# Kernel tuning notes

Hardware: AMD Instinct MI355X
Metric: run time of the kernel (lower is better)

Reference implementation:

```python
import jax, jax.numpy as jnp
import numpy as np

N = 50000   # nodes
E = 800000  # edges before self-loops
H = 4       # heads
D = 64      # num_h_feats (per-head out dim of hidden layers)
C = 2       # num_classes
NEG = 0.2   # DGL GATConv leaky_relu negative_slope
EPS = 1e-5  # BatchNorm eps


def setup_inputs() -> dict:
    key = jax.random.key(0)
    ks = jax.random.split(key, 16)
    inp = {}
    inp['feats'] = jax.random.normal(ks[0], (N, 9), jnp.float32)
    inp['W1'] = jax.random.normal(ks[1], (9, H * D), jnp.float32) * 0.1
    inp['al1'] = jax.random.normal(ks[2], (H, D), jnp.float32) * 0.1
    inp['ar1'] = jax.random.normal(ks[3], (H, D), jnp.float32) * 0.1
    inp['b1'] = jnp.zeros((H, D), jnp.float32)
    inp['Wm'] = jax.random.normal(ks[4], (D, H * D), jnp.float32) * 0.1
    inp['alm'] = jax.random.normal(ks[5], (H, D), jnp.float32) * 0.1
    inp['arm'] = jax.random.normal(ks[6], (H, D), jnp.float32) * 0.1
    inp['bm'] = jnp.zeros((H, D), jnp.float32)
    inp['W2'] = jax.random.normal(ks[7], (D, H * C), jnp.float32) * 0.1
    inp['al2'] = jax.random.normal(ks[8], (H, C), jnp.float32) * 0.1
    inp['ar2'] = jax.random.normal(ks[9], (H, C), jnp.float32) * 0.1
    inp['b2'] = jnp.zeros((H, C), jnp.float32)
    inp['gamma'] = jnp.ones((D,), jnp.float32)
    inp['beta'] = jnp.zeros((D,), jnp.float32)
    inp['src'] = jax.random.randint(ks[10], (E,), 0, N, jnp.int32)
    inp['dst'] = jax.random.randint(ks[11], (E,), 0, N, jnp.int32)
    return inp


def gat_layer(x, W, al, ar, b, src, dst, out_d):
    """DGL GATConv: linear -> per-edge attention -> dst-softmax -> scatter-sum."""
    n = x.shape[0]
    z = (x @ W).reshape(n, H, out_d)                 # [N, H, Dout]
    el = jnp.sum(z * al, axis=-1)                    # [N, H] attn on src
    er = jnp.sum(z * ar, axis=-1)                    # [N, H] attn on dst
    e = jax.nn.leaky_relu(el[src] + er[dst], NEG)    # [E, H]
    m = jax.ops.segment_max(e, dst, num_segments=n)  # per-dst max (stable softmax)
    a = jnp.exp(e - m[dst])
    s = jax.ops.segment_sum(a, dst, num_segments=n)
    alpha = a / s[dst]                               # [E, H]
    out = jax.ops.segment_sum(alpha[:, :, None] * z[src], dst, num_segments=n)
    return out + b                                   # [N, H, Dout]


def batchnorm(h, gamma, beta):
    mu = jnp.mean(h, axis=0)
    var = jnp.var(h, axis=0)
    return (h - mu) * jax.lax.rsqrt(var + EPS) * gamma + beta


def reference(feats, W1, al1, ar1, b1, Wm, alm, arm, bm, W2, al2, ar2, b2,
              gamma, beta, src, dst):
    # dgl.add_self_loop
    loop = jnp.arange(N, dtype=src.dtype)
    s = jnp.concatenate([src, loop])
    d = jnp.concatenate([dst, loop])
    h = gat_layer(feats, W1, al1, ar1, b1, s, d, D).sum(axis=1)  # head-sum
    h = batchnorm(h, gamma, beta)
    h = gat_layer(h, Wm, alm, arm, bm, s, d, D).sum(axis=1)
    h = batchnorm(h, gamma, beta)
    o = gat_layer(h, W2, al2, ar2, b2, s, d, C).sum(axis=1)      # [N, C]
    return o
```

## Files before the change

### kernel.cpp

```cpp
#include <hip/hip_runtime.h>
#include <hip/hip_bf16.h>

typedef __hip_bfloat16 bf16;
typedef __bf16 bf16x8 __attribute__((ext_vector_type(8)));
typedef float f32x4 __attribute__((ext_vector_type(4)));
typedef _Float16 h16;
typedef _Float16 h16x4 __attribute__((ext_vector_type(4)));

__device__ __forceinline__ float b2f(bf16 v) { return __bfloat162float(v); }

__device__ __forceinline__ float ldin(const void* p, size_t i, int isb) {
    return isb ? b2f(((const bf16*)p)[i]) : ((const float*)p)[i];
}
__device__ __forceinline__ unsigned short f2bfbits(float f) {
    bf16 v = __float2bfloat16(f);
    return *(unsigned short*)&v;
}

__global__ __launch_bounds__(256) void prep_kernel(
    const void* __restrict__ feats, const void* __restrict__ W1, const void* __restrict__ Wm,
    const void* __restrict__ al1, const void* __restrict__ ar1,
    const void* __restrict__ alm, const void* __restrict__ arm,
    const unsigned* __restrict__ gbits,
    unsigned short* __restrict__ fpad, unsigned short* __restrict__ W1T,
    unsigned short* __restrict__ WmT,
    float* __restrict__ alf1, float* __restrict__ arf1,
    float* __restrict__ alfm, float* __restrict__ arfm,
    int* __restrict__ flag, int Nn) {
    int isb = (gbits[0] == 0x3F803F80u) ? 1 : 0;
    long t = (long)blockIdx.x * 256 + threadIdx.x;
    if (t == 0) *flag = isb;
    long n64 = (long)Nn * 64;
    if (t < n64) {
        int k = (int)(t & 63); long n = t >> 6;
        fpad[t] = (k < 9) ? f2bfbits(ldin(feats, (size_t)n * 9 + k, isb)) : 0;
    } else if (t < n64 + 16384) {
        long u = t - n64; int n = (int)(u >> 6), k = (int)(u & 63);
        W1T[u] = (k < 9) ? f2bfbits(ldin(W1, (size_t)k * 256 + n, isb)) : 0;
    } else if (t < n64 + 32768) {
        long u = t - n64 - 16384; int n = (int)(u >> 6), k = (int)(u & 63);
        WmT[u] = f2bfbits(ldin(Wm, (size_t)k * 256 + n, isb));
    } else if (t < n64 + 32768 + 256) {
        int u = (int)(t - n64 - 32768);
        alf1[u] = ldin(al1, u, isb); arf1[u] = ldin(ar1, u, isb);
        alfm[u] = ldin(alm, u, isb); arfm[u] = ldin(arm, u, isb);
    }
}

__global__ __launch_bounds__(256) void count_kernel(
    const int* __restrict__ dst, int* __restrict__ deg, int E) {
    int t = blockIdx.x * 256 + threadIdx.x;
    if (t < E) atomicAdd(&deg[dst[t]], 1);
}

__global__ __launch_bounds__(256) void scan1_kernel(
    const int* __restrict__ deg, int* __restrict__ off, int* __restrict__ bsum, int Nn) {
    __shared__ int s[256];
    int t = threadIdx.x, i = blockIdx.x * 256 + t;
    int v = (i < Nn) ? deg[i] : 0;
    s[t] = v; __syncthreads();
#pragma unroll
    for (int o = 1; o < 256; o <<= 1) {
        int a = (t >= o) ? s[t - o] : 0;
        __syncthreads();
        s[t] += a;
        __syncthreads();
    }
    if (i < Nn) off[i] = s[t];
    if (t == 255) bsum[blockIdx.x] = s[255];
}

__global__ __launch_bounds__(256) void scan2_kernel(int* __restrict__ bsum, int NB) {
    __shared__ int s[256];
    int t = threadIdx.x;
    int v = (t < NB) ? bsum[t] : 0;
    s[t] = v; __syncthreads();
#pragma unroll
    for (int o = 1; o < 256; o <<= 1) {
        int a = (t >= o) ? s[t - o] : 0;
        __syncthreads();
        s[t] += a;
        __syncthreads();
    }
    if (t < NB) bsum[t] = s[t] - v;
}

__global__ __launch_bounds__(256) void scan3_kernel(
    const int* __restrict__ deg, int* __restrict__ off, int* __restrict__ cur,
    const int* __restrict__ bsum, int Nn, int E) {
    int i = blockIdx.x * 256 + threadIdx.x;
    if (i < Nn) {
        int ex = off[i] - deg[i] + bsum[i >> 8];
        off[i] = ex;
        cur[i] = ex;
    }
    if (i == 0) off[Nn] = E;
}

__global__ __launch_bounds__(256) void scatter_kernel(
    const int* __restrict__ src, const int* __restrict__ dst,
    int* __restrict__ cur, int* __restrict__ adj, int E) {
    int t = blockIdx.x * 256 + threadIdx.x;
    if (t < E) {
        int p = atomicAdd(&cur[dst[t]], 1);
        adj[p] = src[t];
    }
}

__global__ __launch_bounds__(256) void lin_mfma_l1_kernel(
    const unsigned short* __restrict__ xb, const unsigned short* __restrict__ WT,
    const float* __restrict__ alf, const float* __restrict__ arf,
    h16* __restrict__ zh, float* __restrict__ el, float* __restrict__ er, int Nn) {
    __shared__ h16 zs[16 * 256];
    int w = threadIdx.x >> 6;
    int l = threadIdx.x & 63;
    int quad = l >> 4, lc = l & 15;
    int node0 = blockIdx.x * 16;

    int mrow = node0 + lc; if (mrow >= Nn) mrow = Nn - 1;
    const bf16x8* xa = (const bf16x8*)(xb + (size_t)mrow * 64);
    bf16x8 a0 = xa[quad];
    bf16x8 a1 = xa[quad + 4];

    float pe[4] = {0.f, 0.f, 0.f, 0.f}, pr[4] = {0.f, 0.f, 0.f, 0.f};
    int row0 = quad * 4;
#pragma unroll
    for (int ct = 0; ct < 4; ++ct) {
        int col = w * 64 + ct * 16 + lc;
        const bf16x8* wb = (const bf16x8*)(WT + (size_t)col * 64);
        bf16x8 b0 = wb[quad];
        bf16x8 b1 = wb[quad + 4];
        f32x4 c = {0.f, 0.f, 0.f, 0.f};
        c = __builtin_amdgcn_mfma_f32_16x16x32_bf16(a0, b0, c, 0, 0, 0);
        c = __builtin_amdgcn_mfma_f32_16x16x32_bf16(a1, b1, c, 0, 0, 0);
        float av = alf[col], rv = arf[col];
#pragma unroll
        for (int r = 0; r < 4; ++r) {
            pe[r] = fmaf(c[r], av, pe[r]);
            pr[r] = fmaf(c[r], rv, pr[r]);
            zs[(row0 + r) * 256 + col] = (h16)c[r];
        }
    }
#pragma unroll
    for (int o = 1; o < 16; o <<= 1) {
#pragma unroll
        for (int r = 0; r < 4; ++r) {
            pe[r] += __shfl_xor(pe[r], o);
            pr[r] += __shfl_xor(pr[r], o);
        }
    }
    if (lc == 0) {
#pragma unroll
        for (int r = 0; r < 4; ++r) {
            int n = node0 + row0 + r;
            if (n < Nn) { el[n * 4 + w] = pe[r]; er[n * 4 + w] = pr[r]; }
        }
    }
    __syncthreads();
#pragma unroll
    for (int it = 0; it < 2; ++it) {
        int flat = it * 2048 + threadIdx.x * 8;
        int row = flat >> 8;
        if (node0 + row < Nn)
            *(uint4*)(zh + (size_t)node0 * 256 + flat) = *(const uint4*)(zs + flat);
    }
}

__global__ __launch_bounds__(256) void lin_mfma_bn_kernel(
    const float* __restrict__ x, const float* __restrict__ sc, const float* __restrict__ shb,
    const unsigned short* __restrict__ WT,
    const float* __restrict__ alf, const float* __restrict__ arf,
    h16* __restrict__ zh, float* __restrict__ el, float* __restrict__ er, int Nn) {
    __shared__ h16 zs[16 * 256];
    int w = threadIdx.x >> 6;
    int l = threadIdx.x & 63;
    int quad = l >> 4, lc = l & 15;
    int node0 = blockIdx.x * 16;

    int mrow = node0 + lc; if (mrow >= Nn) mrow = Nn - 1;
    const float* xr = x + (size_t)mrow * 64 + quad * 8;
    float4 f0 = ((const float4*)xr)[0];
    float4 f1 = ((const float4*)xr)[1];
    float4 f2 = ((const float4*)(xr + 32))[0];
    float4 f3 = ((const float4*)(xr + 32))[1];
    float4 s0 = ((const float4*)(sc + quad * 8))[0];
    float4 s1 = ((const float4*)(sc + quad * 8))[1];
    float4 s2 = ((const float4*)(sc + 32 + quad * 8))[0];
    float4 s3 = ((const float4*)(sc + 32 + quad * 8))[1];
    float4 h0 = ((const float4*)(shb + quad * 8))[0];
    float4 h1 = ((const float4*)(shb + quad * 8))[1];
    float4 h2 = ((const float4*)(shb + 32 + quad * 8))[0];
    float4 h3 = ((const float4*)(shb + 32 + quad * 8))[1];

    union { bf16x8 v; unsigned short s[8]; } ua, ub;
    ua.s[0] = f2bfbits(fmaf(f0.x, s0.x, h0.x));
    ua.s[1] = f2bfbits(fmaf(f0.y, s0.y, h0.y));
    ua.s[2] = f2bfbits(fmaf(f0.z, s0.z, h0.z));
    ua.s[3] = f2bfbits(fmaf(f0.w, s0.w, h0.w));
    ua.s[4] = f2bfbits(fmaf(f1.x, s1.x, h1.x));
    ua.s[5] = f2bfbits(fmaf(f1.y, s1.y, h1.y));
    ua.s[6] = f2bfbits(fmaf(f1.z, s1.z, h1.z));
    ua.s[7] = f2bfbits(fmaf(f1.w, s1.w, h1.w));
    ub.s[0] = f2bfbits(fmaf(f2.x, s2.x, h2.x));
    ub.s[1] = f2bfbits(fmaf(f2.y, s2.y, h2.y));
    ub.s[2] = f2bfbits(fmaf(f2.z, s2.z, h2.z));
    ub.s[3] = f2bfbits(fmaf(f2.w, s2.w, h2.w));
    ub.s[4] = f2bfbits(fmaf(f3.x, s3.x, h3.x));
    ub.s[5] = f2bfbits(fmaf(f3.y, s3.y, h3.y));
    ub.s[6] = f2bfbits(fmaf(f3.z, s3.z, h3.z));
    ub.s[7] = f2bfbits(fmaf(f3.w, s3.w, h3.w));
    bf16x8 a0 = ua.v, a1 = ub.v;

    float pe[4] = {0.f, 0.f, 0.f, 0.f}, pr[4] = {0.f, 0.f, 0.f, 0.f};
    int row0 = quad * 4;
#pragma unroll
    for (int ct = 0; ct < 4; ++ct) {
        int col = w * 64 + ct * 16 + lc;
        const bf16x8* wb = (const bf16x8*)(WT + (size_t)col * 64);
        bf16x8 b0 = wb[quad];
        bf16x8 b1 = wb[quad + 4];
        f32x4 c = {0.f, 0.f, 0.f, 0.f};
        c = __builtin_amdgcn_mfma_f32_16x16x32_bf16(a0, b0, c, 0, 0, 0);
        c = __builtin_amdgcn_mfma_f32_16x16x32_bf16(a1, b1, c, 0, 0, 0);
        float av = alf[col], rv = arf[col];
#pragma unroll
        for (int r = 0; r < 4; ++r) {
            pe[r] = fmaf(c[r], av, pe[r]);
            pr[r] = fmaf(c[r], rv, pr[r]);
            zs[(row0 + r) * 256 + col] = (h16)c[r];
        }
    }
#pragma unroll
    for (int o = 1; o < 16; o <<= 1) {
#pragma unroll
        for (int r = 0; r < 4; ++r) {
            pe[r] += __shfl_xor(pe[r], o);
            pr[r] += __shfl_xor(pr[r], o);
        }
    }
    if (lc == 0) {
#pragma unroll
        for (int r = 0; r < 4; ++r) {
            int n = node0 + row0 + r;
            if (n < Nn) { el[n * 4 + w] = pe[r]; er[n * 4 + w] = pr[r]; }
        }
    }
    __syncthreads();
#pragma unroll
    for (int it = 0; it < 2; ++it) {
        int flat = it * 2048 + threadIdx.x * 8;
        int row = flat >> 8;
        if (node0 + row < Nn)
            *(uint4*)(zh + (size_t)node0 * 256 + flat) = *(const uint4*)(zs + flat);
    }
}

__global__ void bn_coef_kernel(
    const float* __restrict__ bnsum, const float* __restrict__ bnsumsq,
    const void* __restrict__ gamma, const void* __restrict__ beta,
    float* __restrict__ sc, float* __restrict__ shb,
    const int* __restrict__ flag, int Nn) {
    int isb = *flag;
    int d = threadIdx.x;
    if (d >= 64) return;
    float inv_n = 1.f / (float)Nn;
    float mu = bnsum[d] * inv_n;
    float var = bnsumsq[d] * inv_n - mu * mu;
    float s = rsqrtf(var + 1e-5f) * ldin(gamma, d, isb);
    sc[d] = s;
    shb[d] = ldin(beta, d, isb) - mu * s;
}

__global__ __launch_bounds__(256) void lin3_kernel(
    const float* __restrict__ x, const float* __restrict__ sc, const float* __restrict__ shb,
    const void* __restrict__ W, const void* __restrict__ al, const void* __restrict__ ar,
    float* __restrict__ zc, float* __restrict__ el, float* __restrict__ er,
    const int* __restrict__ flag, int Nn) {
    int isb = *flag;
    int t = blockIdx.x * 256 + threadIdx.x;
    if (t >= Nn * 4) return;
    int n = t >> 2, h = t & 3;
    const float* xr = x + (size_t)n * 64;
    float a0 = 0.f, a1 = 0.f;
#pragma unroll 8
    for (int k = 0; k < 64; k++) {
        float xn = fmaf(xr[k], sc[k], shb[k]);
        a0 += xn * ldin(W, k * 8 + h * 2 + 0, isb);
        a1 += xn * ldin(W, k * 8 + h * 2 + 1, isb);
    }
    zc[n * 8 + h * 2 + 0] = a0;
    zc[n * 8 + h * 2 + 1] = a1;
    el[t] = a0 * ldin(al, h * 2, isb) + a1 * ldin(al, h * 2 + 1, isb);
    er[t] = a0 * ldin(ar, h * 2, isb) + a1 * ldin(ar, h * 2 + 1, isb);
}

__global__ __launch_bounds__(256) void gat_agg64_kernel(
    const h16* __restrict__ zh, const float* __restrict__ el, const float* __restrict__ er,
    const int* __restrict__ off, const int* __restrict__ adj, const void* __restrict__ bias,
    float* __restrict__ x, float* __restrict__ bnsum, float* __restrict__ bnsumsq,
    const int* __restrict__ flag, int Nn, int total_waves) {
    __shared__ __align__(16) float s_sum[4][64], s_sq[4][64];
    int isb = *flag;
    int tid = threadIdx.x;
    int wv = tid >> 6;
    int l = tid & 63;
    int h = l >> 4, q = l & 15;
    int gw = blockIdx.x * 4 + wv;

    float4 bsl;
    bsl.x = ldin(bias, h * 64 + q * 4 + 0, isb);
    bsl.y = ldin(bias, h * 64 + q * 4 + 1, isb);
    bsl.z = ldin(bias, h * 64 + q * 4 + 2, isb);
    bsl.w = ldin(bias, h * 64 + q * 4 + 3, isb);

    float4 bs = {0.f, 0.f, 0.f, 0.f}, bq = {0.f, 0.f, 0.f, 0.f};

    for (int n = gw; n < Nn; n += total_waves) {
        float er_nh = er[n * 4 + h];
        float e0 = el[n * 4 + h] + er_nh;
        e0 = (e0 > 0.f) ? e0 : 0.2f * e0;
        float w0 = __expf(e0);
        h16x4 zsh = ((const h16x4*)(zh + (size_t)n * 256))[h * 16 + q];
        float4 acc;
        acc.x = w0 * (float)zsh.x; acc.y = w0 * (float)zsh.y;
        acc.z = w0 * (float)zsh.z; acc.w = w0 * (float)zsh.w;
        float lsum = w0;
        int s0 = off[n], s1 = off[n + 1];
        for (int i = s0; i < s1; i += 8) {
            int ss[8];
#pragma unroll
            for (int j = 0; j < 8; j++) {
                int idx = i + j;
                ss[j] = adj[idx < s1 ? idx : s1 - 1];
            }
            float ev[8];
#pragma unroll
            for (int j = 0; j < 8; j++) ev[j] = el[ss[j] * 4 + h];
            h16x4 zv[8];
#pragma unroll
            for (int j = 0; j < 8; j++)
                zv[j] = ((const h16x4*)(zh + (size_t)ss[j] * 256))[h * 16 + q];
#pragma unroll
            for (int j = 0; j < 8; j++) {
                float e = ev[j] + er_nh;
                e = (e > 0.f) ? e : 0.2f * e;
                float w = __expf(e);
                if (i + j >= s1) w = 0.f;
                lsum += w;
                acc.x = fmaf(w, (float)zv[j].x, acc.x);
                acc.y = fmaf(w, (float)zv[j].y, acc.y);
                acc.z = fmaf(w, (float)zv[j].z, acc.z);
                acc.w = fmaf(w, (float)zv[j].w, acc.w);
            }
        }
        float inv = 1.f / lsum;
        float4 r;
        r.x = fmaf(acc.x, inv, bsl.x);
        r.y = fmaf(acc.y, inv, bsl.y);
        r.z = fmaf(acc.z, inv, bsl.z);
        r.w = fmaf(acc.w, inv, bsl.w);
#pragma unroll
        for (int o = 16; o < 64; o <<= 1) {
            r.x += __shfl_xor(r.x, o);
            r.y += __shfl_xor(r.y, o);
            r.z += __shfl_xor(r.z, o);
            r.w += __shfl_xor(r.w, o);
        }
        if (h == 0) {
            ((float4*)(x + (size_t)n * 64))[q] = r;
            bs.x += r.x; bs.y += r.y; bs.z += r.z; bs.w += r.w;
            bq.x = fmaf(r.x, r.x, bq.x); bq.y = fmaf(r.y, r.y, bq.y);
            bq.z = fmaf(r.z, r.z, bq.z); bq.w = fmaf(r.w, r.w, bq.w);
        }
    }
    if (h == 0) {
        ((float4*)&s_sum[wv][0])[q] = bs;
        ((float4*)&s_sq[wv][0])[q] = bq;
    }
    __syncthreads();
    if (tid < 64) {
        float s = s_sum[0][tid] + s_sum[1][tid] + s_sum[2][tid] + s_sum[3][tid];
        float qq = s_sq[0][tid] + s_sq[1][tid] + s_sq[2][tid] + s_sq[3][tid];
        atomicAdd(&bnsum[tid], s);
        atomicAdd(&bnsumsq[tid], qq);
    }
}

__global__ __launch_bounds__(256) void gat_agg2_kernel(
    const float* __restrict__ zc, const float* __restrict__ el, const float* __restrict__ er,
    const int* __restrict__ off, const int* __restrict__ adj, const void* __restrict__ bias,
    void* __restrict__ out, const int* __restrict__ flag, int Nn) {
    int isb = *flag;
    int t = blockIdx.x * 256 + threadIdx.x;
    if (t >= Nn * 4) return;
    int n = t >> 2, h = t & 3;
    float er_nh = er[n * 4 + h];
    float e0 = el[n * 4 + h] + er_nh;
    e0 = (e0 > 0.f) ? e0 : 0.2f * e0;
    float w0 = __expf(e0);
    float lsum = w0;
    float2 zn = ((const float2*)zc)[n * 4 + h];
    float a0 = w0 * zn.x, a1 = w0 * zn.y;
    int s0 = off[n], s1 = off[n + 1];
    for (int i = s0; i < s1; i += 4) {
        int ss[4];
#pragma unroll
        for (int j = 0; j < 4; j++) {
            int idx = i + j; if (idx >= s1) idx = s1 - 1;
            ss[j] = adj[idx];
        }
        float ev[4]; float2 zj[4];
#pragma unroll
        for (int j = 0; j < 4; j++) {
            ev[j] = el[ss[j] * 4 + h];
            zj[j] = ((const float2*)zc)[ss[j] * 4 + h];
        }
#pragma unroll
        for (int j = 0; j < 4; j++) {
            float e = ev[j] + er_nh;
            e = (e > 0.f) ? e : 0.2f * e;
            float w = __expf(e);
            if (i + j >= s1) w = 0.f;
            lsum += w;
            a0 = fmaf(w, zj[j].x, a0);
            a1 = fmaf(w, zj[j].y, a1);
        }
    }
    float inv = 1.f / lsum;
    float v0 = fmaf(a0, inv, ldin(bias, h * 2 + 0, isb));
    float v1 = fmaf(a1, inv, ldin(bias, h * 2 + 1, isb));
#pragma unroll
    for (int o = 1; o < 4; o <<= 1) {
        v0 += __shfl_xor(v0, o);
        v1 += __shfl_xor(v1, o);
    }
    if (h == 0) {
        if (isb) {
            ((bf16*)out)[n * 2 + 0] = __float2bfloat16(v0);
            ((bf16*)out)[n * 2 + 1] = __float2bfloat16(v1);
        } else {
            ((float*)out)[n * 2 + 0] = v0;
            ((float*)out)[n * 2 + 1] = v1;
        }
    }
}

extern "C" void kernel_launch(void* const* d_in, const int* in_sizes, int n_in,
                              void* d_out, int out_size, void* d_ws, size_t ws_size,
                              hipStream_t stream) {
    const void* feats = d_in[0];
    const void* W1    = d_in[1];
    const void* al1   = d_in[2];
    const void* ar1   = d_in[3];
    const void* b1    = d_in[4];
    const void* Wm    = d_in[5];
    const void* alm   = d_in[6];
    const void* arm   = d_in[7];
    const void* bm    = d_in[8];
    const void* W2    = d_in[9];
    const void* al2   = d_in[10];
    const void* ar2   = d_in[11];
    const void* b2v   = d_in[12];
    const void* gamma = d_in[13];
    const void* beta  = d_in[14];
    const int*  src   = (const int*)d_in[15];
    const int*  dst   = (const int*)d_in[16];

    int Nn = in_sizes[0] / 9;
    int E  = in_sizes[15];

    float* ws = (float*)d_ws;
    h16*   zh   = (h16*)ws;
    float* zc   = ws + (size_t)Nn * 128;
    float* el   = zc + (size_t)Nn * 8;
    float* er   = el + (size_t)Nn * 4;
    float* x    = er + (size_t)Nn * 4;
    int*   deg  = (int*)(x + (size_t)Nn * 64);
    float* bns1 = (float*)(deg + Nn);
    float* bnq1 = bns1 + 64;
    float* bns2 = bnq1 + 64;
    float* bnq2 = bns2 + 64;
    size_t msetBytes = (size_t)Nn * 4 + 256 * 4;
    float* sc1  = bnq2 + 64;
    float* shb1 = sc1 + 64;
    float* sc2  = shb1 + 64;
    float* shb2 = sc2 + 64;
    float* alf1 = shb2 + 64;
    float* arf1 = alf1 + 256;
    float* alfm = arf1 + 256;
    float* arfm = alfm + 256;
    unsigned short* fpad = (unsigned short*)(arfm + 256);
    unsigned short* W1T  = fpad + (size_t)Nn * 64;
    unsigned short* WmT  = W1T + 256 * 64;
    int*   flag = (int*)(WmT + 256 * 64);
    int*   off  = flag + 1;
    int*   cur  = off + Nn + 1;
    int*   adj  = cur + Nn;
    int*   bsum = adj + E;

    dim3 B(256);
    int NB1 = (Nn + 255) / 256;
    int gE  = (E + 255) / 256;
    int gMF = (Nn + 15) / 16;
    int gN4 = (Nn * 4 + 255) / 256;
    long prepN = (long)Nn * 64 + 32768 + 256;
    int gPrep = (int)((prepN + 255) / 256);
    int AGG_GRID = 2048;
    int total_waves = AGG_GRID * 4;

    prep_kernel<<<gPrep, B, 0, stream>>>(feats, W1, Wm, al1, ar1, alm, arm,
                                         (const unsigned*)gamma, fpad, W1T, WmT,
                                         alf1, arf1, alfm, arfm, flag, Nn);

    hipMemsetAsync(deg, 0, msetBytes, stream);
    count_kernel<<<gE, B, 0, stream>>>(dst, deg, E);
    scan1_kernel<<<NB1, B, 0, stream>>>(deg, off, bsum, Nn);
    scan2_kernel<<<1, B, 0, stream>>>(bsum, NB1);
    scan3_kernel<<<NB1, B, 0, stream>>>(deg, off, cur, bsum, Nn, E);
    scatter_kernel<<<gE, B, 0, stream>>>(src, dst, cur, adj, E);

    lin_mfma_l1_kernel<<<gMF, B, 0, stream>>>(fpad, W1T, alf1, arf1, zh, el, er, Nn);
    gat_agg64_kernel<<<AGG_GRID, B, 0, stream>>>(
        zh, el, er, off, adj, b1, x, bns1, bnq1, flag, Nn, total_waves);
    bn_coef_kernel<<<1, 64, 0, stream>>>(bns1, bnq1, gamma, beta, sc1, shb1, flag, Nn);

    lin_mfma_bn_kernel<<<gMF, B, 0, stream>>>(x, sc1, shb1, WmT, alfm, arfm, zh, el, er, Nn);
    gat_agg64_kernel<<<AGG_GRID, B, 0, stream>>>(
        zh, el, er, off, adj, bm, x, bns2, bnq2, flag, Nn, total_waves);
    bn_coef_kernel<<<1, 64, 0, stream>>>(bns2, bnq2, gamma, beta, sc2, shb2, flag, Nn);

    lin3_kernel<<<gN4, B, 0, stream>>>(x, sc2, shb2, W2, al2, ar2, zc, el, er, flag, Nn);
    gat_agg2_kernel<<<gN4, B, 0, stream>>>(zc, el, er, off, adj, b2v, d_out, flag, Nn);
}
```

Before: 465.1 us.

## Software-pipeline GAT aggregation gathers, use exp2 with prescaled logits, split BN stats

The 64-wide aggregation kernel now double-buffers neighbour index loads and feature/logit gathers in groups of four, and prefetches the next node's offsets and logits so load latency overlaps compute. Attention logits are prescaled by log2(e) so the hardware exp2 can be used. Padded edges point at a sentinel node whose logit is -1e30 and whose features are zero, which removes the per-edge masks. BatchNorm statistics move out of the aggregation kernel into a separate reduction kernel. This costs an extra launch and a re-read of x, and relies on the sentinel padding rows being written correctly.

```diff
diff --git a/kernel.cpp b/kernel.cpp
--- a/kernel.cpp
+++ b/kernel.cpp
@@ -6,6 +6,8 @@
 typedef float f32x4 __attribute__((ext_vector_type(4)));
 typedef _Float16 h16;
 typedef _Float16 h16x4 __attribute__((ext_vector_type(4)));
+
+#define LOG2E 1.44269504088896340736f
 
 __device__ __forceinline__ float b2f(bf16 v) { return __bfloat162float(v); }
 
@@ -26,6 +28,7 @@
     unsigned short* __restrict__ WmT,
     float* __restrict__ alf1, float* __restrict__ arf1,
     float* __restrict__ alfm, float* __restrict__ arfm,
+    unsigned short* __restrict__ zhs, float* __restrict__ zcs, float* __restrict__ elp,
     int* __restrict__ flag, int Nn) {
     int isb = (gbits[0] == 0x3F803F80u) ? 1 : 0;
     long t = (long)blockIdx.x * 256 + threadIdx.x;
@@ -42,8 +45,17 @@
         WmT[u] = f2bfbits(ldin(Wm, (size_t)k * 256 + n, isb));
     } else if (t < n64 + 32768 + 256) {
         int u = (int)(t - n64 - 32768);
-        alf1[u] = ldin(al1, u, isb); arf1[u] = ldin(ar1, u, isb);
-        alfm[u] = ldin(alm, u, isb); arfm[u] = ldin(arm, u, isb);
+        alf1[u] = ldin(al1, u, isb) * LOG2E; arf1[u] = ldin(ar1, u, isb) * LOG2E;
+        alfm[u] = ldin(alm, u, isb) * LOG2E; arfm[u] = ldin(arm, u, isb) * LOG2E;
+    } else {
+        long u = t - (n64 + 32768 + 256);
+        if (u < 4) {
+            elp[(size_t)Nn * 4 + u] = -1e30f;
+        } else if (u < 260) {
+            zhs[(size_t)Nn * 256 + (u - 4)] = 0;
+        } else if (u < 268) {
+            zcs[(size_t)Nn * 8 + (u - 260)] = 0.f;
+        }
     }
 }
 
@@ -255,6 +267,29 @@
     }
 }
 
+__global__ __launch_bounds__(256) void bnstats_kernel(
+    const float* __restrict__ x, float* __restrict__ bnsum, float* __restrict__ bnsumsq,
+    int Nn) {
+    __shared__ float ssum[4][64], ssq[4][64];
+    int tid = threadIdx.x;
+    int d = tid & 63, r = tid >> 6;
+    float s = 0.f, q = 0.f;
+    int stride = gridDim.x * 4;
+    for (int n = blockIdx.x * 4 + r; n < Nn; n += stride) {
+        float v = x[(size_t)n * 64 + d];
+        s += v;
+        q = fmaf(v, v, q);
+    }
+    ssum[r][d] = s; ssq[r][d] = q;
+    __syncthreads();
+    if (tid < 64) {
+        float ts = ssum[0][tid] + ssum[1][tid] + ssum[2][tid] + ssum[3][tid];
+        float tq = ssq[0][tid] + ssq[1][tid] + ssq[2][tid] + ssq[3][tid];
+        atomicAdd(&bnsum[tid], ts);
+        atomicAdd(&bnsumsq[tid], tq);
+    }
+}
+
 __global__ void bn_coef_kernel(
     const float* __restrict__ bnsum, const float* __restrict__ bnsumsq,
     const void* __restrict__ gamma, const void* __restrict__ beta,
@@ -290,69 +325,105 @@
     }
     zc[n * 8 + h * 2 + 0] = a0;
     zc[n * 8 + h * 2 + 1] = a1;
-    el[t] = a0 * ldin(al, h * 2, isb) + a1 * ldin(al, h * 2 + 1, isb);
-    er[t] = a0 * ldin(ar, h * 2, isb) + a1 * ldin(ar, h * 2 + 1, isb);
-}
+    el[t] = (a0 * ldin(al, h * 2, isb) + a1 * ldin(al, h * 2 + 1, isb)) * LOG2E;
+    er[t] = (a0 * ldin(ar, h * 2, isb) + a1 * ldin(ar, h * 2 + 1, isb)) * LOG2E;
+}
+
+#define LDADJ(dstv, bidx)                                   \
+    {                                                       \
+        _Pragma("unroll") for (int j = 0; j < 4; j++) {     \
+            int idx = (bidx) + j;                           \
+            int ok = idx < s1;                              \
+            int v = adj[ok ? idx : s0];                     \
+            dstv[j] = ok ? v : Nn;                          \
+        }                                                   \
+    }
+#define ISSUE(ev, zv, ss)                                                          \
+    {                                                                              \
+        _Pragma("unroll") for (int j = 0; j < 4; j++) ev[j] = el[ss[j] * 4 + h];   \
+        _Pragma("unroll") for (int j = 0; j < 4; j++)                              \
+            zv[j] = zrow[(size_t)ss[j] * 64 + l];                                  \
+    }
+#define COMPUTE(ev, zv)                                     \
+    {                                                       \
+        _Pragma("unroll") for (int j = 0; j < 4; j++) {     \
+            float e = ev[j] + ern;                          \
+            e = fmaxf(e, 0.2f * e);                         \
+            float wj = __builtin_amdgcn_exp2f(e);           \
+            lsum += wj;                                     \
+            acc.x = fmaf(wj, (float)zv[j].x, acc.x);        \
+            acc.y = fmaf(wj, (float)zv[j].y, acc.y);        \
+            acc.z = fmaf(wj, (float)zv[j].z, acc.z);        \
+            acc.w = fmaf(wj, (float)zv[j].w, acc.w);        \
+        }                                                   \
+    }
 
 __global__ __launch_bounds__(256) void gat_agg64_kernel(
     const h16* __restrict__ zh, const float* __restrict__ el, const float* __restrict__ er,
     const int* __restrict__ off, const int* __restrict__ adj, const void* __restrict__ bias,
-    float* __restrict__ x, float* __restrict__ bnsum, float* __restrict__ bnsumsq,
-    const int* __restrict__ flag, int Nn, int total_waves) {
-    __shared__ __align__(16) float s_sum[4][64], s_sq[4][64];
+    float* __restrict__ x, const int* __restrict__ flag, int Nn, int total_waves) {
     int isb = *flag;
     int tid = threadIdx.x;
-    int wv = tid >> 6;
     int l = tid & 63;
-    int h = l >> 4, q = l & 15;
-    int gw = blockIdx.x * 4 + wv;
+    int h = l >> 4;
+    int gw = blockIdx.x * 4 + (tid >> 6);
+    const h16x4* zrow = (const h16x4*)zh;
 
     float4 bsl;
-    bsl.x = ldin(bias, h * 64 + q * 4 + 0, isb);
-    bsl.y = ldin(bias, h * 64 + q * 4 + 1, isb);
-    bsl.z = ldin(bias, h * 64 + q * 4 + 2, isb);
-    bsl.w = ldin(bias, h * 64 + q * 4 + 3, isb);
-
-    float4 bs = {0.f, 0.f, 0.f, 0.f}, bq = {0.f, 0.f, 0.f, 0.f};
-
-    for (int n = gw; n < Nn; n += total_waves) {
-        float er_nh = er[n * 4 + h];
-        float e0 = el[n * 4 + h] + er_nh;
-        e0 = (e0 > 0.f) ? e0 : 0.2f * e0;
-        float w0 = __expf(e0);
-        h16x4 zsh = ((const h16x4*)(zh + (size_t)n * 256))[h * 16 + q];
-        float4 acc;
-        acc.x = w0 * (float)zsh.x; acc.y = w0 * (float)zsh.y;
-        acc.z = w0 * (float)zsh.z; acc.w = w0 * (float)zsh.w;
+    bsl.x = ldin(bias, l * 4 + 0, isb);
+    bsl.y = ldin(bias, l * 4 + 1, isb);
+    bsl.z = ldin(bias, l * 4 + 2, isb);
+    bsl.w = ldin(bias, l * 4 + 3, isb);
+
+    if (gw >= Nn) return;
+
+    int n = gw;
+    int fs0 = off[n], fs1 = off[n + 1];
+    float fel = el[n * 4 + h], fer = er[n * 4 + h];
+
+    while (true) {
+        int s0 = fs0, s1 = fs1;
+        float eln = fel, ern = fer;
+        h16x4 zself = zrow[(size_t)n * 64 + l];
+        int nn = n + total_waves;
+        if (nn < Nn) {
+            fs0 = off[nn]; fs1 = off[nn + 1];
+            fel = el[nn * 4 + h]; fer = er[nn * 4 + h];
+        }
+
+        float e0 = eln + ern;
+        e0 = fmaxf(e0, 0.2f * e0);
+        float w0 = __builtin_amdgcn_exp2f(e0);
         float lsum = w0;
-        int s0 = off[n], s1 = off[n + 1];
-        for (int i = s0; i < s1; i += 8) {
-            int ss[8];
-#pragma unroll
-            for (int j = 0; j < 8; j++) {
-                int idx = i + j;
-                ss[j] = adj[idx < s1 ? idx : s1 - 1];
+        float4 acc = {0.f, 0.f, 0.f, 0.f};
+
+        int deg = s1 - s0;
+        if (deg > 0) {
+            int nb = (deg + 3) >> 2;
+            int sA[4], sB[4];
+            float evA[4], evB[4];
+            h16x4 zvA[4], zvB[4];
+            LDADJ(sA, s0);
+            ISSUE(evA, zvA, sA);
+            if (nb > 1) LDADJ(sB, s0 + 4);
+            int k = 0;
+            while (true) {
+                if (k + 1 < nb) ISSUE(evB, zvB, sB);
+                if (k + 2 < nb) LDADJ(sA, s0 + (k + 2) * 4);
+                COMPUTE(evA, zvA);
+                if (++k >= nb) break;
+                if (k + 1 < nb) ISSUE(evA, zvA, sA);
+                if (k + 2 < nb) LDADJ(sB, s0 + (k + 2) * 4);
+                COMPUTE(evB, zvB);
+                if (++k >= nb) break;
             }
-            float ev[8];
-#pragma unroll
-            for (int j = 0; j < 8; j++) ev[j] = el[ss[j] * 4 + h];
-            h16x4 zv[8];
-#pragma unroll
-            for (int j = 0; j < 8; j++)
-                zv[j] = ((const h16x4*)(zh + (size_t)ss[j] * 256))[h * 16 + q];
-#pragma unroll
-            for (int j = 0; j < 8; j++) {
-                float e = ev[j] + er_nh;
-                e = (e > 0.f) ? e : 0.2f * e;
-                float w = __expf(e);
-                if (i + j >= s1) w = 0.f;
-                lsum += w;
-                acc.x = fmaf(w, (float)zv[j].x, acc.x);
-                acc.y = fmaf(w, (float)zv[j].y, acc.y);
-                acc.z = fmaf(w, (float)zv[j].z, acc.z);
-                acc.w = fmaf(w, (float)zv[j].w, acc.w);
-            }
-        }
+        }
+
+        acc.x = fmaf(w0, (float)zself.x, acc.x);
+        acc.y = fmaf(w0, (float)zself.y, acc.y);
+        acc.z = fmaf(w0, (float)zself.z, acc.z);
+        acc.w = fmaf(w0, (float)zself.w, acc.w);
+
         float inv = 1.f / lsum;
         float4 r;
         r.x = fmaf(acc.x, inv, bsl.x);
@@ -366,25 +437,14 @@
             r.z += __shfl_xor(r.z, o);
             r.w += __shfl_xor(r.w, o);
         }
-        if (h == 0) {
-            ((float4*)(x + (size_t)n * 64))[q] = r;
-            bs.x += r.x; bs.y += r.y; bs.z += r.z; bs.w += r.w;
-            bq.x = fmaf(r.x, r.x, bq.x); bq.y = fmaf(r.y, r.y, bq.y);
-            bq.z = fmaf(r.z, r.z, bq.z); bq.w = fmaf(r.w, r.w, bq.w);
-        }
-    }
-    if (h == 0) {
-        ((float4*)&s_sum[wv][0])[q] = bs;
-        ((float4*)&s_sq[wv][0])[q] = bq;
-    }
-    __syncthreads();
-    if (tid < 64) {
-        float s = s_sum[0][tid] + s_sum[1][tid] + s_sum[2][tid] + s_sum[3][tid];
-        float qq = s_sq[0][tid] + s_sq[1][tid] + s_sq[2][tid] + s_sq[3][tid];
-        atomicAdd(&bnsum[tid], s);
-        atomicAdd(&bnsumsq[tid], qq);
-    }
-}
+        if (h == 0) ((float4*)(x + (size_t)n * 64))[l & 15] = r;
+        if (nn >= Nn) break;
+        n = nn;
+    }
+}
+#undef LDADJ
+#undef ISSUE
+#undef COMPUTE
 
 __global__ __launch_bounds__(256) void gat_agg2_kernel(
     const float* __restrict__ zc, const float* __restrict__ el, const float* __restrict__ er,
@@ -396,8 +456,8 @@
     int n = t >> 2, h = t & 3;
     float er_nh = er[n * 4 + h];
     float e0 = el[n * 4 + h] + er_nh;
-    e0 = (e0 > 0.f) ? e0 : 0.2f * e0;
-    float w0 = __expf(e0);
+    e0 = fmaxf(e0, 0.2f * e0);
+    float w0 = __builtin_amdgcn_exp2f(e0);
     float lsum = w0;
     float2 zn = ((const float2*)zc)[n * 4 + h];
     float a0 = w0 * zn.x, a1 = w0 * zn.y;
@@ -406,8 +466,10 @@
         int ss[4];
 #pragma unroll
         for (int j = 0; j < 4; j++) {
-            int idx = i + j; if (idx >= s1) idx = s1 - 1;
-            ss[j] = adj[idx];
+            int idx = i + j;
+            int ok = idx < s1;
+            int v = adj[ok ? idx : s0];
+            ss[j] = ok ? v : Nn;
         }
         float ev[4]; float2 zj[4];
 #pragma unroll
@@ -418,9 +480,8 @@
 #pragma unroll
         for (int j = 0; j < 4; j++) {
             float e = ev[j] + er_nh;
-            e = (e > 0.f) ? e : 0.2f * e;
-            float w = __expf(e);
-            if (i + j >= s1) w = 0.f;
+            e = fmaxf(e, 0.2f * e);
+            float w = __builtin_amdgcn_exp2f(e);
             lsum += w;
             a0 = fmaf(w, zj[j].x, a0);
             a1 = fmaf(w, zj[j].y, a1);
@@ -471,9 +532,9 @@
 
     float* ws = (float*)d_ws;
     h16*   zh   = (h16*)ws;
-    float* zc   = ws + (size_t)Nn * 128;
-    float* el   = zc + (size_t)Nn * 8;
-    float* er   = el + (size_t)Nn * 4;
+    float* zc   = ws + (size_t)Nn * 128 + 128;
+    float* el   = zc + (size_t)Nn * 8 + 8;
+    float* er   = el + (size_t)Nn * 4 + 4;
     float* x    = er + (size_t)Nn * 4;
     int*   deg  = (int*)(x + (size_t)Nn * 64);
     float* bns1 = (float*)(deg + Nn);
@@ -503,14 +564,15 @@
     int gE  = (E + 255) / 256;
     int gMF = (Nn + 15) / 16;
     int gN4 = (Nn * 4 + 255) / 256;
-    long prepN = (long)Nn * 64 + 32768 + 256;
+    long prepN = (long)Nn * 64 + 32768 + 256 + 268;
     int gPrep = (int)((prepN + 255) / 256);
     int AGG_GRID = 2048;
     int total_waves = AGG_GRID * 4;
 
     prep_kernel<<<gPrep, B, 0, stream>>>(feats, W1, Wm, al1, ar1, alm, arm,
                                          (const unsigned*)gamma, fpad, W1T, WmT,
-                                         alf1, arf1, alfm, arfm, flag, Nn);
+                                         alf1, arf1, alfm, arfm,
+                                         (unsigned short*)zh, zc, el, flag, Nn);
 
     hipMemsetAsync(deg, 0, msetBytes, stream);
     count_kernel<<<gE, B, 0, stream>>>(dst, deg, E);
@@ -521,12 +583,14 @@
 
     lin_mfma_l1_kernel<<<gMF, B, 0, stream>>>(fpad, W1T, alf1, arf1, zh, el, er, Nn);
     gat_agg64_kernel<<<AGG_GRID, B, 0, stream>>>(
-        zh, el, er, off, adj, b1, x, bns1, bnq1, flag, Nn, total_waves);
+        zh, el, er, off, adj, b1, x, flag, Nn, total_waves);
+    bnstats_kernel<<<512, B, 0, stream>>>(x, bns1, bnq1, Nn);
     bn_coef_kernel<<<1, 64, 0, stream>>>(bns1, bnq1, gamma, beta, sc1, shb1, flag, Nn);
 
     lin_mfma_bn_kernel<<<gMF, B, 0, stream>>>(x, sc1, shb1, WmT, alfm, arfm, zh, el, er, Nn);
     gat_agg64_kernel<<<AGG_GRID, B, 0, stream>>>(
-        zh, el, er, off, adj, bm, x, bns2, bnq2, flag, Nn, total_waves);
+        zh, el, er, off, adj, bm, x, flag, Nn, total_waves);
+    bnstats_kernel<<<512, B, 0, stream>>>(x, bns2, bnq2, Nn);
     bn_coef_kernel<<<1, 64, 0, stream>>>(bns2, bnq2, gamma, beta, sc2, shb2, flag, Nn);
 
     lin3_kernel<<<gN4, B, 0, stream>>>(x, sc2, shb2, W2, al2, ar2, zc, el, er, flag, Nn);
```

After: 465.2 us. Within noise of the previous version (+0.0%).
